# Kernel tuning notes

Measured on AMD Instinct MI355X. Metric: run time of the kernel, lower is better.

## Reference

```python
import jax, jax.numpy as jnp
import numpy as np
from jax import lax

B, N, T, E = 16, 2048, 48, 32
C0, C1 = 64, 64
H1, H2 = 256, 128
NPRED = 12
KT = 3
SCALE = float(np.sqrt(C1))


def setup_inputs() -> dict:
    key = jax.random.key(0)
    ks = jax.random.split(key, 20)
    def lin(k, fin, fout):
        bound = 1.0 / np.sqrt(fin)
        kw, kb = jax.random.split(k)
        W = jax.random.uniform(kw, (fin, fout), jnp.float32, -bound, bound)
        b = jax.random.uniform(kb, (fout,), jnp.float32, -bound, bound)
        return W, b
    x = jax.random.normal(ks[0], (B, N, T, E), jnp.float32)
    W_in, b_in = lin(ks[1], E, C0)
    # conv kernel laid out WIO for lax.conv_general_dilated ('NWC','WIO','NWC')
    bound = 1.0 / np.sqrt(C0 * KT)
    W_conv = jax.random.uniform(ks[2], (KT, C0, C1), jnp.float32, -bound, bound)
    b_conv = jax.random.uniform(ks[3], (C1,), jnp.float32, -bound, bound)
    Wq, bq = lin(ks[4], C1, C1)
    Wk, bk = lin(ks[5], C1, C1)
    Wv, bv = lin(ks[6], C1, C1)
    W1, b1 = lin(ks[7], C1, H1)
    W2, b2 = lin(ks[8], H1, H2)
    W3, b3 = lin(ks[9], H2, NPRED)
    return dict(x=x, W_in=W_in, b_in=b_in, W_conv=W_conv, b_conv=b_conv,
                Wq=Wq, bq=bq, Wk=Wk, bk=bk, Wv=Wv, bv=bv,
                W1=W1, b1=b1, W2=W2, b2=b2, W3=W3, b3=b3)


def reference(x, W_in, b_in, W_conv, b_conv, Wq, bq, Wk, bk, Wv, bv,
              W1, b1, W2, b2, W3, b3):
    Bs, Ns, Ts, Es = x.shape
    # input linear, fold nodes into batch (weights shared across nodes)
    h = jnp.einsum('bnte,ec->bntc', x, W_in) + b_in          # [B,N,T,C0]
    h = h.reshape(Bs * Ns, Ts, C0)                            # [BN,T,C0]
    # temporal conv over T, kernel KT, pad 1 each side (matches Conv2d (Kt,1), pad (1,0))
    h = lax.conv_general_dilated(h, W_conv, window_strides=(1,),
                                 padding=[(1, 1)],
                                 dimension_numbers=('NWC', 'WIO', 'NWC')) + b_conv
    h = jax.nn.relu(h)                                        # [BN,T,C1]
    q = h @ Wq + bq
    k = h @ Wk + bk
    v = h @ Wv + bv
    scores = jnp.einsum('btd,bsd->bts', q, k) / SCALE         # [BN,T,T]
    attn = jax.nn.softmax(scores, axis=-1)
    ctx = jnp.einsum('bts,bsd->btd', attn, v)                 # [BN,T,C1]
    last = ctx[:, -1, :]                                      # [BN,C1]
    # output MLP (dropout is identity in eval/reference)
    z = jax.nn.relu(last @ W1 + b1)
    z = jax.nn.relu(z @ W2 + b2)
    pred = z @ W3 + b3                                        # [BN,NPRED]
    out = pred.reshape(Bs, Ns, NPRED)                         # [B,N,P]
    out = jnp.transpose(out, (0, 2, 1))[:, None]              # [B,1,P,N]
    return out
```

## Files before the change

### kernel.cpp

```cpp
#include <hip/hip_runtime.h>
#include <hip/hip_bf16.h>
#include <math.h>

#define TT 48
#define NSEQ (16*2048)
#define NP 12

typedef __bf16 bf16x8 __attribute__((ext_vector_type(8)));
typedef float  f32x4  __attribute__((ext_vector_type(4)));

#define OFF_WCC 0
#define OFF_MQK 6144
#define OFF_WV  10240
#define OFF_W1  18432
#define OFF_W2  34816
#define WS_BTOT 33792
#define WS_BC0  33856
#define WS_BC2  33920
#define WS_KV0  33984
#define WS_CTX  34048

__device__ __forceinline__ f32x4 zero4() {
  f32x4 z; z[0] = 0.f; z[1] = 0.f; z[2] = 0.f; z[3] = 0.f; return z;
}

union PackU { bf16x8 v; __hip_bfloat162 h[4]; };

__device__ __forceinline__ bf16x8 pack8(float4 a, float4 b) {
  PackU u;
  u.h[0] = __float22bfloat162_rn(make_float2(a.x, a.y));
  u.h[1] = __float22bfloat162_rn(make_float2(a.z, a.w));
  u.h[2] = __float22bfloat162_rn(make_float2(b.x, b.y));
  u.h[3] = __float22bfloat162_rn(make_float2(b.z, b.w));
  return u.v;
}

__global__ __launch_bounds__(256) void prep_kernel(
    const float* __restrict__ W_in, const float* __restrict__ b_in,
    const float* __restrict__ W_conv, const float* __restrict__ b_conv,
    const float* __restrict__ Wk, const float* __restrict__ Wv,
    const float* __restrict__ Wq, const float* __restrict__ bq,
    const float* __restrict__ W1, const float* __restrict__ W2,
    float* __restrict__ ws)
{
  __bf16* wsb = (__bf16*)ws;
  const int tid = threadIdx.x;
  const int bid = blockIdx.x;
  if (bid < 24) {
    int gid = bid * 256 + tid;
    int kk = gid >> 6;
    int c  = gid & 63;
    int dt = kk >> 5;
    int e  = kk & 31;
    const float* wrow = W_in + e * 64;
    const float* wc   = W_conv + dt * 4096 + c;
    float acc = 0.f;
    #pragma unroll 8
    for (int c0 = 0; c0 < 64; ++c0)
      acc = fmaf(wrow[c0], wc[c0 * 64], acc);
    wsb[OFF_WCC + ((kk >> 3) * 64 + c) * 8 + (kk & 7)] = (__bf16)acc;
  } else if (bid < 40) {
    int gid = (bid - 24) * 256 + tid;
    int d = gid >> 6, c = gid & 63;
    const float* qr = Wq + d * 64;
    const float* kr = Wk + c * 64;
    float acc = 0.f;
    #pragma unroll 8
    for (int j = 0; j < 64; ++j) acc = fmaf(qr[j], kr[j], acc);
    wsb[OFF_MQK + ((d >> 3) * 64 + c) * 8 + (d & 7)] = (__bf16)(0.125f * acc);
  } else if (bid < 56) {
    int gid = (bid - 40) * 256 + tid;
    int kk = gid >> 6, c = gid & 63;
    wsb[OFF_WV + ((kk >> 3) * 64 + c) * 8 + (kk & 7)] = (__bf16)Wv[kk * 64 + c];
  } else if (bid < 120) {
    int gid = (bid - 56) * 256 + tid;
    int kk = gid >> 8, n = gid & 255;
    wsb[OFF_W1 + ((kk >> 3) * 256 + n) * 8 + (kk & 7)] = (__bf16)W1[kk * 256 + n];
  } else if (bid < 248) {
    int gid = (bid - 120) * 256 + tid;
    int kk = gid >> 7, n = gid & 127;
    wsb[OFF_W2 + ((kk >> 3) * 128 + n) * 8 + (kk & 7)] = (__bf16)W2[kk * 128 + n];
  } else if (tid < 64) {
    int c = tid;
    float s[3];
    for (int dt = 0; dt < 3; ++dt) {
      const float* wc = W_conv + dt * 4096 + c;
      float a = 0.f;
      for (int c0 = 0; c0 < 64; ++c0) a = fmaf(b_in[c0], wc[c0 * 64], a);
      s[dt] = a;
    }
    ws[WS_BC0 + c]  = s[0];
    ws[WS_BC2 + c]  = s[2];
    ws[WS_BTOT + c] = s[0] + s[1] + s[2] + b_conv[c];
    float a = 0.f;
    const float* kr = Wk + c * 64;
    for (int j = 0; j < 64; ++j) a = fmaf(kr[j], bq[j], a);
    ws[WS_KV0 + c] = 0.125f * a;
  }
}

__global__ __launch_bounds__(128, 4) void attn_kernel(
    const float* __restrict__ x, const float* __restrict__ bv,
    const float* __restrict__ ws, float* __restrict__ ctx)
{
  __shared__ __bf16 h1s[2][48 * 66];
  __shared__ __bf16 wbufs[2][64];

  const int tid  = threadIdx.x;
  const int lane = tid & 63;
  const int wv   = tid >> 6;
  const int m16  = lane & 15;
  const int quad = lane >> 4;
  const int seq  = blockIdx.x * 2 + wv;
  __bf16* h1   = h1s[wv];
  __bf16* wbuf = wbufs[wv];

  const __bf16* wsb  = (const __bf16*)ws;
  const bf16x8* WccB = (const bf16x8*)(wsb + OFF_WCC);
  const bf16x8* MqkB = (const bf16x8*)(wsb + OFF_MQK);
  const bf16x8* WvB  = (const bf16x8*)(wsb + OFF_WV);
  const float*  wsf  = ws;
  const float*  xseq = x + (size_t)seq * (TT * 32);

  float4 xa[3][3], xb[3][3];
  #pragma unroll
  for (int mt = 0; mt < 3; ++mt)
    #pragma unroll
    for (int ks = 0; ks < 3; ++ks) {
      const int tg = mt * 16 + m16 + ks - 1;
      const int tc = tg < 0 ? 0 : (tg > 47 ? 47 : tg);
      const float* ap = xseq + tc * 32 + quad * 8;
      xa[mt][ks] = *(const float4*)ap;
      xb[mt][ks] = *(const float4*)(ap + 4);
    }

  float bt_[2][2], b0_[2][2], b2_[2][2];
  #pragma unroll
  for (int nh = 0; nh < 2; ++nh)
    #pragma unroll
    for (int j = 0; j < 2; ++j) {
      const int c = nh * 32 + j * 16 + m16;
      bt_[nh][j] = wsf[WS_BTOT + c];
      b0_[nh][j] = wsf[WS_BC0 + c];
      b2_[nh][j] = wsf[WS_BC2 + c];
    }
  float kv0_[4];
  #pragma unroll
  for (int nt = 0; nt < 4; ++nt) kv0_[nt] = wsf[WS_KV0 + nt * 16 + m16];

  bf16x8 af[3][3];
  #pragma unroll
  for (int mt = 0; mt < 3; ++mt)
    #pragma unroll
    for (int ks = 0; ks < 3; ++ks) {
      if ((mt == 0 && ks == 0) || (mt == 2 && ks == 2)) {
        const int tg = mt * 16 + m16 + ks - 1;
        const bool ok = (tg >= 0 && tg < 48);
        bf16x8 z8;
        #pragma unroll
        for (int j = 0; j < 8; ++j) z8[j] = (__bf16)0.f;
        af[mt][ks] = ok ? pack8(xa[mt][ks], xb[mt][ks]) : z8;
      } else {
        af[mt][ks] = pack8(xa[mt][ks], xb[mt][ks]);
      }
    }

  #pragma unroll
  for (int nh = 0; nh < 2; ++nh) {
    bf16x8 bfr[3][2];
    #pragma unroll
    for (int ks = 0; ks < 3; ++ks) {
      bfr[ks][0] = WccB[(ks * 4 + quad) * 64 + nh * 32 + m16];
      bfr[ks][1] = WccB[(ks * 4 + quad) * 64 + nh * 32 + 16 + m16];
    }
    f32x4 acc[3][2];
    #pragma unroll
    for (int mt = 0; mt < 3; ++mt) { acc[mt][0] = zero4(); acc[mt][1] = zero4(); }
    #pragma unroll
    for (int ks = 0; ks < 3; ++ks) {
      #pragma unroll
      for (int mt = 0; mt < 3; ++mt) {
        acc[mt][0] = __builtin_amdgcn_mfma_f32_16x16x32_bf16(af[mt][ks], bfr[ks][0], acc[mt][0], 0, 0, 0);
        acc[mt][1] = __builtin_amdgcn_mfma_f32_16x16x32_bf16(af[mt][ks], bfr[ks][1], acc[mt][1], 0, 0, 0);
      }
    }
    #pragma unroll
    for (int j = 0; j < 2; ++j) {
      const int c = nh * 32 + j * 16 + m16;
      const float bt  = bt_[nh][j];
      const float b0v = b0_[nh][j];
      const float b2v = b2_[nh][j];
      #pragma unroll
      for (int mt = 0; mt < 3; ++mt)
        #pragma unroll
        for (int r = 0; r < 4; ++r) {
          const int trow = mt * 16 + quad * 4 + r;
          float v = acc[mt][j][r] + bt;
          if (mt == 0 && r == 0 && quad == 0) v -= b0v;
          if (mt == 2 && r == 3 && quad == 3) v -= b2v;
          h1[trow * 66 + c] = (__bf16)fmaxf(v, 0.f);
        }
    }
  }
  __asm__ __volatile__("s_waitcnt lgkmcnt(0)" ::: "memory");

  bf16x8 a8[3][2];
  #pragma unroll
  for (int mt = 0; mt < 3; ++mt)
    #pragma unroll
    for (int ks = 0; ks < 2; ++ks)
      a8[mt][ks] = *(const bf16x8*)&h1[(mt * 16 + m16) * 66 + ks * 32 + quad * 8];

  {
    bf16x8 mq[2][4];
    #pragma unroll
    for (int ks = 0; ks < 2; ++ks)
      #pragma unroll
      for (int nt = 0; nt < 4; ++nt)
        mq[ks][nt] = MqkB[(ks * 4 + quad) * 64 + nt * 16 + m16];
    f32x4 qa[4] = {zero4(), zero4(), zero4(), zero4()};
    #pragma unroll
    for (int ks = 0; ks < 2; ++ks)
      #pragma unroll
      for (int nt = 0; nt < 4; ++nt)
        qa[nt] = __builtin_amdgcn_mfma_f32_16x16x32_bf16(
            a8[2][ks], mq[ks][nt], qa[nt], 0, 0, 0);
    if (quad == 3) {
      #pragma unroll
      for (int nt = 0; nt < 4; ++nt)
        wbuf[nt * 16 + m16] = (__bf16)(qa[nt][3] + kv0_[nt]);
    }
  }
  __asm__ __volatile__("s_waitcnt lgkmcnt(0)" ::: "memory");

  float p[3][4];
  {
    bf16x8 wB0 = *(const bf16x8*)&wbuf[quad * 8];
    bf16x8 wB1 = *(const bf16x8*)&wbuf[32 + quad * 8];
    f32x4 sa[3] = {zero4(), zero4(), zero4()};
    #pragma unroll
    for (int mt = 0; mt < 3; ++mt) {
      sa[mt] = __builtin_amdgcn_mfma_f32_16x16x32_bf16(a8[mt][0], wB0, sa[mt], 0, 0, 0);
      sa[mt] = __builtin_amdgcn_mfma_f32_16x16x32_bf16(a8[mt][1], wB1, sa[mt], 0, 0, 0);
    }
    float mx = -INFINITY;
    #pragma unroll
    for (int mt = 0; mt < 3; ++mt)
      #pragma unroll
      for (int r = 0; r < 4; ++r) mx = fmaxf(mx, sa[mt][r]);
    mx = fmaxf(mx, __shfl_xor(mx, 16, 64));
    mx = fmaxf(mx, __shfl_xor(mx, 32, 64));
    float l = 0.f;
    #pragma unroll
    for (int mt = 0; mt < 3; ++mt)
      #pragma unroll
      for (int r = 0; r < 4; ++r) {
        float e = __expf(sa[mt][r] - mx);
        p[mt][r] = e;
        l += e;
      }
    l += __shfl_xor(l, 16, 64);
    l += __shfl_xor(l, 32, 64);
    float rl = 1.f / l;
    #pragma unroll
    for (int mt = 0; mt < 3; ++mt)
      #pragma unroll
      for (int r = 0; r < 4; ++r) p[mt][r] *= rl;
  }

  {
    float cx[4];
    #pragma unroll
    for (int nh = 0; nh < 2; ++nh) {
      bf16x8 vb[2][2];
      #pragma unroll
      for (int ks = 0; ks < 2; ++ks) {
        vb[ks][0] = WvB[(ks * 4 + quad) * 64 + nh * 32 + m16];
        vb[ks][1] = WvB[(ks * 4 + quad) * 64 + nh * 32 + 16 + m16];
      }
      f32x4 va[3][2];
      #pragma unroll
      for (int mt = 0; mt < 3; ++mt) { va[mt][0] = zero4(); va[mt][1] = zero4(); }
      #pragma unroll
      for (int ks = 0; ks < 2; ++ks) {
        #pragma unroll
        for (int mt = 0; mt < 3; ++mt) {
          va[mt][0] = __builtin_amdgcn_mfma_f32_16x16x32_bf16(a8[mt][ks], vb[ks][0], va[mt][0], 0, 0, 0);
          va[mt][1] = __builtin_amdgcn_mfma_f32_16x16x32_bf16(a8[mt][ks], vb[ks][1], va[mt][1], 0, 0, 0);
        }
      }
      #pragma unroll
      for (int j = 0; j < 2; ++j) {
        float a = 0.f;
        #pragma unroll
        for (int mt = 0; mt < 3; ++mt)
          #pragma unroll
          for (int r = 0; r < 4; ++r)
            a = fmaf(p[mt][r], va[mt][j][r], a);
        cx[nh * 2 + j] = a;
      }
    }
    #pragma unroll
    for (int nt = 0; nt < 4; ++nt) {
      cx[nt] += __shfl_xor(cx[nt], 16, 64);
      cx[nt] += __shfl_xor(cx[nt], 32, 64);
    }
    if (quad == 0) {
      #pragma unroll
      for (int nt = 0; nt < 4; ++nt)
        ctx[(size_t)seq * 64 + nt * 16 + m16] = cx[nt] + bv[nt * 16 + m16];
    }
  }
}

__global__ __launch_bounds__(256) void mlp_kernel(
    const float* __restrict__ ctx, const float* __restrict__ ws,
    const float* __restrict__ b1, const float* __restrict__ b2,
    const float* __restrict__ W3, const float* __restrict__ b3,
    float* __restrict__ out)
{
  __shared__ __bf16 Xs[16 * 68];
  __shared__ __bf16 z1[16 * 264];
  __shared__ float  z2[16 * 132];

  const int tid  = threadIdx.x;
  const int r0   = blockIdx.x * 16;
  const int lane = tid & 63;
  const int wv   = tid >> 6;
  const int m16  = lane & 15;
  const int quad = lane >> 4;

  const __bf16* wsb = (const __bf16*)ws;
  const bf16x8* W1B = (const bf16x8*)(wsb + OFF_W1);
  const bf16x8* W2B = (const bf16x8*)(wsb + OFF_W2);

  {
    int row = tid >> 4, c4 = (tid & 15) * 4;
    float4 a = *(const float4*)(ctx + (size_t)(r0 + row) * 64 + c4);
    __bf16* d = &Xs[row * 68 + c4];
    d[0] = (__bf16)a.x; d[1] = (__bf16)a.y; d[2] = (__bf16)a.z; d[3] = (__bf16)a.w;
  }
  __syncthreads();

  {
    bf16x8 a8[2];
    #pragma unroll
    for (int ks = 0; ks < 2; ++ks)
      a8[ks] = *(const bf16x8*)&Xs[m16 * 68 + ks * 32 + quad * 8];
    f32x4 acc[4] = {zero4(), zero4(), zero4(), zero4()};
    #pragma unroll
    for (int nt = 0; nt < 4; ++nt) {
      int n = wv * 64 + nt * 16 + m16;
      #pragma unroll
      for (int ks = 0; ks < 2; ++ks)
        acc[nt] = __builtin_amdgcn_mfma_f32_16x16x32_bf16(
            a8[ks], W1B[(ks * 4 + quad) * 256 + n], acc[nt], 0, 0, 0);
    }
    #pragma unroll
    for (int nt = 0; nt < 4; ++nt) {
      int n = wv * 64 + nt * 16 + m16;
      float bb = b1[n];
      #pragma unroll
      for (int r = 0; r < 4; ++r)
        z1[(quad * 4 + r) * 264 + n] = (__bf16)fmaxf(acc[nt][r] + bb, 0.f);
    }
  }
  __syncthreads();

  {
    f32x4 acc[2] = {zero4(), zero4()};
    #pragma unroll 2
    for (int ks = 0; ks < 8; ++ks) {
      bf16x8 a = *(const bf16x8*)&z1[m16 * 264 + ks * 32 + quad * 8];
      #pragma unroll
      for (int nt = 0; nt < 2; ++nt)
        acc[nt] = __builtin_amdgcn_mfma_f32_16x16x32_bf16(
            a, W2B[(ks * 4 + quad) * 128 + wv * 32 + nt * 16 + m16], acc[nt], 0, 0, 0);
    }
    #pragma unroll
    for (int nt = 0; nt < 2; ++nt) {
      int n = wv * 32 + nt * 16 + m16;
      float bb = b2[n];
      #pragma unroll
      for (int r = 0; r < 4; ++r)
        z2[(quad * 4 + r) * 132 + n] = fmaxf(acc[nt][r] + bb, 0.f);
    }
  }
  __syncthreads();

  if (tid < 16 * NP) {
    int r = tid / NP, pp = tid - r * NP;
    const float* zr = z2 + r * 132;
    float a0 = b3[pp], a1 = 0.f, a2 = 0.f, a3 = 0.f;
    #pragma unroll 8
    for (int k = 0; k < 128; k += 4) {
      float4 f = *(const float4*)(zr + k);
      a0 = fmaf(f.x, W3[k * NP + pp],       a0);
      a1 = fmaf(f.y, W3[(k + 1) * NP + pp], a1);
      a2 = fmaf(f.z, W3[(k + 2) * NP + pp], a2);
      a3 = fmaf(f.w, W3[(k + 3) * NP + pp], a3);
    }
    float a = (a0 + a1) + (a2 + a3);
    int row = r0 + r;
    int bb = row >> 11, nn = row & 2047;
    out[(size_t)bb * (NP * 2048) + pp * 2048 + nn] = a;
  }
}

extern "C" void kernel_launch(void* const* d_in, const int* in_sizes, int n_in,
                              void* d_out, int out_size, void* d_ws, size_t ws_size,
                              hipStream_t stream) {
  const float* x      = (const float*)d_in[0];
  const float* W_in   = (const float*)d_in[1];
  const float* b_in   = (const float*)d_in[2];
  const float* W_conv = (const float*)d_in[3];
  const float* b_conv = (const float*)d_in[4];
  const float* Wq     = (const float*)d_in[5];
  const float* bq     = (const float*)d_in[6];
  const float* Wk     = (const float*)d_in[7];
  const float* bk     = (const float*)d_in[8];  (void)bk;
  const float* Wv     = (const float*)d_in[9];
  const float* bv     = (const float*)d_in[10];
  const float* W1     = (const float*)d_in[11];
  const float* b1     = (const float*)d_in[12];
  const float* W2     = (const float*)d_in[13];
  const float* b2     = (const float*)d_in[14];
  const float* W3     = (const float*)d_in[15];
  const float* b3     = (const float*)d_in[16];
  float* ws  = (float*)d_ws;
  float* out = (float*)d_out;

  prep_kernel<<<249, 256, 0, stream>>>(W_in, b_in, W_conv, b_conv, Wk, Wv, Wq, bq, W1, W2, ws);
  attn_kernel<<<NSEQ / 2, 128, 0, stream>>>(x, bv, ws, ws + WS_CTX);
  mlp_kernel<<<NSEQ / 16, 256, 0, stream>>>(ws + WS_CTX, ws, b1, b2, W3, b3, out);
}
```

Measured before the change: 366.6 us.

## Stage x through LDS as bf16 with coalesced loads, pad h1 rows, raise occupancy

Each sequence's x tile is now loaded with six fully coalesced float4 loads per lane, converted once to bf16 and staged in shared memory (80-byte row stride). The 9 MFMA A-fragments are then read back from LDS, replacing 18 redundant, overlapping global float4 loads and 9 pack conversions. The h1 row stride is padded from 66 to 72 bf16, which makes the 16-byte fragment reads aligned and reuses the same buffer for x staging. The launch-bounds occupancy hint rises from 4 to 6 blocks per CU, which may constrain registers and cause spills.

```diff
diff --git a/kernel.cpp b/kernel.cpp
--- a/kernel.cpp
+++ b/kernel.cpp
@@ -25,6 +25,7 @@
 }
 
 union PackU { bf16x8 v; __hip_bfloat162 h[4]; };
+union Pack4 { unsigned long long u; __hip_bfloat162 h[2]; };
 
 __device__ __forceinline__ bf16x8 pack8(float4 a, float4 b) {
   PackU u;
@@ -33,6 +34,13 @@
   u.h[2] = __float22bfloat162_rn(make_float2(b.x, b.y));
   u.h[3] = __float22bfloat162_rn(make_float2(b.z, b.w));
   return u.v;
+}
+
+__device__ __forceinline__ unsigned long long pack4(float4 a) {
+  Pack4 u;
+  u.h[0] = __float22bfloat162_rn(make_float2(a.x, a.y));
+  u.h[1] = __float22bfloat162_rn(make_float2(a.z, a.w));
+  return u.u;
 }
 
 __global__ __launch_bounds__(256) void prep_kernel(
@@ -99,11 +107,11 @@
   }
 }
 
-__global__ __launch_bounds__(128, 4) void attn_kernel(
+__global__ __launch_bounds__(128, 6) void attn_kernel(
     const float* __restrict__ x, const float* __restrict__ bv,
     const float* __restrict__ ws, float* __restrict__ ctx)
 {
-  __shared__ __bf16 h1s[2][48 * 66];
+  __shared__ __align__(16) __bf16 h1s[2][48 * 72];
   __shared__ __bf16 wbufs[2][64];
 
   const int tid  = threadIdx.x;
@@ -114,6 +122,7 @@
   const int seq  = blockIdx.x * 2 + wv;
   __bf16* h1   = h1s[wv];
   __bf16* wbuf = wbufs[wv];
+  char* xt = (char*)h1;
 
   const __bf16* wsb  = (const __bf16*)ws;
   const bf16x8* WccB = (const bf16x8*)(wsb + OFF_WCC);
@@ -122,17 +131,12 @@
   const float*  wsf  = ws;
   const float*  xseq = x + (size_t)seq * (TT * 32);
 
-  float4 xa[3][3], xb[3][3];
-  #pragma unroll
-  for (int mt = 0; mt < 3; ++mt)
-    #pragma unroll
-    for (int ks = 0; ks < 3; ++ks) {
-      const int tg = mt * 16 + m16 + ks - 1;
-      const int tc = tg < 0 ? 0 : (tg > 47 ? 47 : tg);
-      const float* ap = xseq + tc * 32 + quad * 8;
-      xa[mt][ks] = *(const float4*)ap;
-      xb[mt][ks] = *(const float4*)(ap + 4);
-    }
+  float4 xg0 = *(const float4*)(xseq + (lane +   0) * 4);
+  float4 xg1 = *(const float4*)(xseq + (lane +  64) * 4);
+  float4 xg2 = *(const float4*)(xseq + (lane + 128) * 4);
+  float4 xg3 = *(const float4*)(xseq + (lane + 192) * 4);
+  float4 xg4 = *(const float4*)(xseq + (lane + 256) * 4);
+  float4 xg5 = *(const float4*)(xseq + (lane + 320) * 4);
 
   float bt_[2][2], b0_[2][2], b2_[2][2];
   #pragma unroll
@@ -148,20 +152,32 @@
   #pragma unroll
   for (int nt = 0; nt < 4; ++nt) kv0_[nt] = wsf[WS_KV0 + nt * 16 + m16];
 
+  {
+    #define XSTORE(i, g) { \
+      const int c_ = lane + 64 * (i); \
+      *(unsigned long long*)(xt + (c_ >> 3) * 80 + (c_ & 7) * 8) = pack4(g); }
+    XSTORE(0, xg0) XSTORE(1, xg1) XSTORE(2, xg2)
+    XSTORE(3, xg3) XSTORE(4, xg4) XSTORE(5, xg5)
+    #undef XSTORE
+  }
+  __asm__ __volatile__("s_waitcnt lgkmcnt(0)" ::: "memory");
+
   bf16x8 af[3][3];
   #pragma unroll
   for (int mt = 0; mt < 3; ++mt)
     #pragma unroll
     for (int ks = 0; ks < 3; ++ks) {
+      const int tg = mt * 16 + m16 + ks - 1;
+      const int rc = tg < 0 ? 0 : (tg > 47 ? 47 : tg);
+      bf16x8 v = *(const bf16x8*)(xt + rc * 80 + quad * 16);
       if ((mt == 0 && ks == 0) || (mt == 2 && ks == 2)) {
-        const int tg = mt * 16 + m16 + ks - 1;
         const bool ok = (tg >= 0 && tg < 48);
         bf16x8 z8;
         #pragma unroll
         for (int j = 0; j < 8; ++j) z8[j] = (__bf16)0.f;
-        af[mt][ks] = ok ? pack8(xa[mt][ks], xb[mt][ks]) : z8;
+        af[mt][ks] = ok ? v : z8;
       } else {
-        af[mt][ks] = pack8(xa[mt][ks], xb[mt][ks]);
+        af[mt][ks] = v;
       }
     }
 
@@ -198,7 +214,7 @@
           float v = acc[mt][j][r] + bt;
           if (mt == 0 && r == 0 && quad == 0) v -= b0v;
           if (mt == 2 && r == 3 && quad == 3) v -= b2v;
-          h1[trow * 66 + c] = (__bf16)fmaxf(v, 0.f);
+          h1[trow * 72 + c] = (__bf16)fmaxf(v, 0.f);
         }
     }
   }
@@ -209,7 +225,7 @@
   for (int mt = 0; mt < 3; ++mt)
     #pragma unroll
     for (int ks = 0; ks < 2; ++ks)
-      a8[mt][ks] = *(const bf16x8*)&h1[(mt * 16 + m16) * 66 + ks * 32 + quad * 8];
+      a8[mt][ks] = *(const bf16x8*)&h1[(mt * 16 + m16) * 72 + ks * 32 + quad * 8];
 
   {
     bf16x8 mq[2][4];
```

Result: slower. 416.6 us (+13.6%).
